# Kernel tuning notes

Hardware: AMD Instinct MI355X
Metric: run time of the kernel (lower is better)

## Reference

```python
import jax, jax.numpy as jnp
import numpy as np

B, N, C = 4, 1024, 768
H = 12
D = C // H
SCALE = D ** -0.5


def setup_inputs() -> dict:
    key = jax.random.key(0)
    k1, k2, k3, k4, k5 = jax.random.split(key, 5)
    inp = {
        'input': jax.random.normal(k1, (B, N, C), dtype=jnp.float32),
        'input_jvp': jax.random.normal(k2, (B, N, C), dtype=jnp.float32),
        # qkv linear (no bias), proj linear (with bias), torch Linear layout [out, in]
        'W_qkv': jax.random.normal(k3, (3 * C, C), dtype=jnp.float32) * (C ** -0.5),
        'W_proj': jax.random.normal(k4, (C, C), dtype=jnp.float32) * (C ** -0.5),
        'b_proj': jax.random.normal(k5, (C,), dtype=jnp.float32) * 0.02,
    }
    return inp


def _split_heads(t):
    t = t.reshape(B, N, 3, H, D).transpose(2, 0, 3, 1, 4)
    return t[0], t[1], t[2]


def reference(input, input_jvp, W_qkv, W_proj, b_proj):
    # LinearLinear: primal gets full affine, tangent gets linear part only
    qkv = jnp.einsum('bnc,oc->bno', input, W_qkv)
    qkv_jvp = jnp.einsum('bnc,oc->bno', input_jvp, W_qkv)
    q, k, v = _split_heads(qkv)
    q_jvp, k_jvp, v_jvp = _split_heads(qkv_jvp)

    q = q * SCALE
    attn = jax.nn.softmax(jnp.einsum('bhnd,bhmd->bhnm', q, k), axis=-1)
    x = jnp.einsum('bhnm,bhmd->bhnd', attn, v)

    q_jvp = q_jvp * SCALE
    A_jvp = jnp.einsum('bhnd,bhmd->bhnm', q_jvp, k)
    B_jvp = jnp.einsum('bhnd,bhmd->bhnm', q, k_jvp)
    C_jvp = jnp.einsum('bhnm,bhmd->bhnd', attn, v_jvp)
    dm_by_dr = A_jvp + B_jvp
    # softmax JVP: attn * (dm - rowsum(dm * attn))
    attn_filter_1 = dm_by_dr * attn
    row = jnp.sum(dm_by_dr * attn, axis=-1, keepdims=True)  # = diag(dm @ attn^T)
    attn_filter = attn_filter_1 - row * attn
    x_jvp = jnp.einsum('bhnm,bhmd->bhnd', attn_filter, v) + C_jvp

    x = x.transpose(0, 2, 1, 3).reshape(B, N, C)
    x_jvp = x_jvp.transpose(0, 2, 1, 3).reshape(B, N, C)

    x = jnp.einsum('bnc,oc->bno', x, W_proj) + b_proj
    x_jvp = jnp.einsum('bnc,oc->bno', x_jvp, W_proj)
    return (x, x_jvp)
```

## Files before the change

### kernel.cpp

```cpp
#include <hip/hip_runtime.h>

constexpr int Bn = 4;
constexpr int Nn = 1024;
constexpr int Cn = 768;
constexpr int Hn = 12;
constexpr int Dn = 64;
constexpr float SCALE_Q = 0.125f;
constexpr int SEG = Bn * Nn * Cn;
constexpr int NDn = Nn * Dn;
constexpr int WQ_ELE = 3 * Cn * Cn;
constexpr int WP_ELE = Cn * Cn;

typedef __attribute__((ext_vector_type(8))) short bf16x8;
typedef __attribute__((ext_vector_type(4))) float f32x4;

__device__ __forceinline__ unsigned short f2bf(float f) {
    union { float f; unsigned u; } v; v.f = f;
    unsigned r = v.u + 0x7fffu + ((v.u >> 16) & 1u);
    return (unsigned short)(r >> 16);
}
__device__ __forceinline__ float bf2f(unsigned short b) {
    union { unsigned u; float f; } v; v.u = ((unsigned)b) << 16;
    return v.f;
}
__device__ __forceinline__ bf16x8 ldfrag(const unsigned short* base, int boff) {
    return *(const bf16x8*)((const char*)base + boff);
}
#define MFMA(a, b, c) __builtin_amdgcn_mfma_f32_16x16x32_bf16((a), (b), (c), 0, 0, 0)


__global__ __launch_bounds__(256)
void conv_k(const float* __restrict__ a0, const float* __restrict__ a1,
            unsigned short* __restrict__ dst)
{
    const int P = SEG / 4;
    const int j = blockIdx.x * 256 + threadIdx.x;
    const int arr = j / P;
    const int i = (j - arr * P) * 4;
    const float* __restrict__ src = arr ? a1 : a0;
    const float4 f = *(const float4*)(src + i);
    const float ff[4] = {f.x, f.y, f.z, f.w};
    ushort4 h, lo;
#pragma unroll
    for (int t = 0; t < 4; ++t) {
        const unsigned short hv = f2bf(ff[t]);
        (&h.x)[t] = hv;
        (&lo.x)[t] = f2bf(ff[t] - bf2f(hv));
    }
    *(ushort4*)(dst + (size_t)(2 * arr) * SEG + i) = h;
    *(ushort4*)(dst + (size_t)(2 * arr + 1) * SEG + i) = lo;
}

__global__ __launch_bounds__(256)
void conv_w(const float* __restrict__ src, unsigned short* __restrict__ dh,
            unsigned short* __restrict__ dl)
{
    const int i = (blockIdx.x * 256 + threadIdx.x) * 4;
    const float4 f = *(const float4*)(src + i);
    const float ff[4] = {f.x, f.y, f.z, f.w};
    ushort4 h, lo;
#pragma unroll
    for (int t = 0; t < 4; ++t) {
        const unsigned short hv = f2bf(ff[t]);
        (&h.x)[t] = hv;
        (&lo.x)[t] = f2bf(ff[t] - bf2f(hv));
    }
    *(ushort4*)(dh + i) = h;
    *(ushort4*)(dl + i) = lo;
}

template<int MODE>
__global__ __launch_bounds__(256, 2)
void gemm_mfma(const unsigned short* __restrict__ Abase,
               const unsigned short* __restrict__ Wh,
               const unsigned short* __restrict__ Wl,
               const float* __restrict__ bias,
               unsigned short* __restrict__ qkv, float* __restrict__ out)
{
    __shared__ unsigned short sAh[128 * 64];
    __shared__ unsigned short sAl[128 * 64];
    __shared__ unsigned short sBh[128 * 64];
    __shared__ unsigned short sBl[128 * 64];

    const int tid = threadIdx.x;
    const int z = blockIdx.z;
    const int row0 = blockIdx.y << 7;
    const int col0 = blockIdx.x << 7;
    const int l = tid & 63, w = tid >> 6;
    const int wr = w >> 1, wc = w & 1;
    const int h4 = l >> 4, l15 = l & 15;
    const int sw = (l15 & 7) << 4;
    const int srow = tid >> 3;
    const int ss = tid & 7;

    const unsigned short* __restrict__ Ah = Abase + (size_t)(2 * z) * SEG;
    const unsigned short* __restrict__ Al = Abase + (size_t)(2 * z + 1) * SEG;

    f32x4 acc[4][4];
#pragma unroll
    for (int m = 0; m < 4; ++m)
#pragma unroll
        for (int n = 0; n < 4; ++n)
            acc[m][n] = (f32x4){0.f, 0.f, 0.f, 0.f};

    bf16x8 pAh[4], pAl[4], pBh[4], pBl[4];

#define G_LOADT(K0_) {                                                        \
    _Pragma("unroll")                                                         \
    for (int it = 0; it < 4; ++it) {                                          \
        const int row = srow + 32 * it;                                       \
        const size_t goA = (size_t)(row0 + row) * Cn + (K0_) + 8 * ss;        \
        const size_t goB = (size_t)(col0 + row) * Cn + (K0_) + 8 * ss;        \
        pAh[it] = *(const bf16x8*)(Ah + goA);                                 \
        pAl[it] = *(const bf16x8*)(Al + goA);                                 \
        pBh[it] = *(const bf16x8*)(Wh + goB);                                 \
        pBl[it] = *(const bf16x8*)(Wl + goB);                                 \
    } }

    G_LOADT(0);

    for (int k0 = 0; k0 < Cn; k0 += 64) {
        __syncthreads();
#pragma unroll
        for (int it = 0; it < 4; ++it) {
            const int row = srow + 32 * it;
            const int boff = row * 128 + ((ss ^ (row & 7)) << 4);
            *(bf16x8*)((char*)sAh + boff) = pAh[it];
            *(bf16x8*)((char*)sAl + boff) = pAl[it];
            *(bf16x8*)((char*)sBh + boff) = pBh[it];
            *(bf16x8*)((char*)sBl + boff) = pBl[it];
        }
        const int kn = (k0 + 64 < Cn) ? k0 + 64 : 0;
        G_LOADT(kn);
        __syncthreads();
#pragma unroll
        for (int c = 0; c < 2; ++c) {
            bf16x8 ah[4], al[4], bh[4], bl[4];
#pragma unroll
            for (int m = 0; m < 4; ++m) {
                const int boff = (64 * wr + 16 * m + l15) * 128 + ((((c << 2) | h4) << 4) ^ sw);
                ah[m] = ldfrag(sAh, boff);
                al[m] = ldfrag(sAl, boff);
            }
#pragma unroll
            for (int n = 0; n < 4; ++n) {
                const int boff = (64 * wc + 16 * n + l15) * 128 + ((((c << 2) | h4) << 4) ^ sw);
                bh[n] = ldfrag(sBh, boff);
                bl[n] = ldfrag(sBl, boff);
            }
#pragma unroll
            for (int m = 0; m < 4; ++m)
#pragma unroll
                for (int n = 0; n < 4; ++n) {
                    acc[m][n] = MFMA(ah[m], bh[n], acc[m][n]);
                    acc[m][n] = MFMA(ah[m], bl[n], acc[m][n]);
                    acc[m][n] = MFMA(al[m], bh[n], acc[m][n]);
                }
        }
    }

    if (MODE == 0) {
#pragma unroll
        for (int n = 0; n < 4; ++n) {
            const int colb = col0 + 64 * wc + 16 * n;
            const int t = colb / Cn;
            const int rem = colb - t * Cn;
            const int hh = rem >> 6;
            const int d = (rem & 63) + l15;
            const float sc = (t == 0) ? SCALE_Q : 1.0f;
            const int t2 = t + 3 * z;
            unsigned short* __restrict__ dh = qkv + (size_t)(2 * t2) * SEG;
            unsigned short* __restrict__ dl = dh + SEG;
#pragma unroll
            for (int m = 0; m < 4; ++m)
#pragma unroll
                for (int r = 0; r < 4; ++r) {
                    const int row = row0 + 64 * wr + 16 * m + 4 * h4 + r;
                    const int b = row >> 10, nq = row & 1023;
                    const size_t ad = (size_t)(b * Hn + hh) * NDn +
                        (t == 2 ? (size_t)d * Nn + nq
                                : (size_t)nq * 64 + d);
                    const float vv = acc[m][n][r] * sc;
                    const unsigned short hv = f2bf(vv);
                    dh[ad] = hv;
                    dl[ad] = f2bf(vv - bf2f(hv));
                }
        }
    } else {
#pragma unroll
        for (int n = 0; n < 4; ++n) {
            const int col = col0 + 64 * wc + 16 * n + l15;
            const float bi = (z == 0) ? bias[col] : 0.0f;
#pragma unroll
            for (int m = 0; m < 4; ++m)
#pragma unroll
                for (int r = 0; r < 4; ++r) {
                    const int row = row0 + 64 * wr + 16 * m + 4 * h4 + r;
                    out[(size_t)z * SEG + (size_t)row * Cn + col] = acc[m][n][r] + bi;
                }
        }
    }
}

__global__ __launch_bounds__(256, 2)
void attn_mfma(unsigned short* __restrict__ wsu)
{
    __shared__ unsigned short sKV[4][64 * 64];
    __shared__ unsigned short sP[4][4][16 * 64];

    const int tid = threadIdx.x;
    const int l = tid & 63;
    const int w = tid >> 6;
    const int h4 = l >> 4;
    const int l15 = l & 15;
    const int sw = (l15 & 7) << 4;
    const int rA = tid >> 3;
    const int ss = tid & 7;
    const int rB = rA + 32;

    const int bh = blockIdx.x;
    const int r0 = blockIdx.y << 6;

    const unsigned short* __restrict__ Bq = wsu + 4 * (size_t)SEG + (size_t)bh * NDn;
    const unsigned short* __restrict__ qh   = Bq;
    const unsigned short* __restrict__ kh   = Bq + 2 * (size_t)SEG;
    const unsigned short* __restrict__ vth  = Bq + 4 * (size_t)SEG;
    const unsigned short* __restrict__ qjh  = Bq + 6 * (size_t)SEG;
    const unsigned short* __restrict__ kjh  = Bq + 8 * (size_t)SEG;
    const unsigned short* __restrict__ vjth = Bq + 10 * (size_t)SEG;

    bf16x8 qhi[2], qlo[2], qjhi[2], qjlo[2];
    {
        const int qrow = r0 + w * 16 + l15;
#pragma unroll
        for (int c = 0; c < 2; ++c) {
            const size_t o = (size_t)qrow * 64 + c * 32 + h4 * 8;
            qhi[c] = *(const bf16x8*)(qh + o);
            qlo[c] = *(const bf16x8*)(qh + SEG + o);
            qjhi[c] = *(const bf16x8*)(qjh + o);
            qjlo[c] = *(const bf16x8*)(qjh + SEG + o);
        }
    }

    f32x4 mold = {-3.0e38f, -3.0e38f, -3.0e38f, -3.0e38f};
    f32x4 l_run = {0.f, 0.f, 0.f, 0.f};
    f32x4 ar_run = {0.f, 0.f, 0.f, 0.f};
    f32x4 ax[4], ac[4], ad[4];
#pragma unroll
    for (int ds = 0; ds < 4; ++ds) {
        ax[ds] = (f32x4){0.f, 0.f, 0.f, 0.f};
        ac[ds] = (f32x4){0.f, 0.f, 0.f, 0.f};
        ad[ds] = (f32x4){0.f, 0.f, 0.f, 0.f};
    }

    bf16x8 kr0[4], kr1[4], vr0[4], vr1[4];
    const int ba = rA * 128 + ((ss ^ (rA & 7)) << 4);
    const int bb = rB * 128 + ((ss ^ (rA & 7)) << 4);

#define A_LOADK(JT_) {                                                         \
    const size_t ga = (size_t)((JT_) + rA) * 64 + 8 * ss;                      \
    const size_t gb = (size_t)((JT_) + rB) * 64 + 8 * ss;                      \
    kr0[0] = *(const bf16x8*)(kh + ga);        kr1[0] = *(const bf16x8*)(kh + gb); \
    kr0[1] = *(const bf16x8*)(kh + SEG + ga);  kr1[1] = *(const bf16x8*)(kh + SEG + gb); \
    kr0[2] = *(const bf16x8*)(kjh + ga);       kr1[2] = *(const bf16x8*)(kjh + gb); \
    kr0[3] = *(const bf16x8*)(kjh + SEG + ga); kr1[3] = *(const bf16x8*)(kjh + SEG + gb); }

#define A_LOADV(JT_) {                                                         \
    const size_t ga = (size_t)rA * Nn + (JT_) + 8 * ss;                        \
    const size_t gb = (size_t)rB * Nn + (JT_) + 8 * ss;                        \
    vr0[0] = *(const bf16x8*)(vth + ga);        vr1[0] = *(const bf16x8*)(vth + gb); \
    vr0[1] = *(const bf16x8*)(vth + SEG + ga);  vr1[1] = *(const bf16x8*)(vth + SEG + gb); \
    vr0[2] = *(const bf16x8*)(vjth + ga);       vr1[2] = *(const bf16x8*)(vjth + gb); \
    vr0[3] = *(const bf16x8*)(vjth + SEG + ga); vr1[3] = *(const bf16x8*)(vjth + SEG + gb); }

#define A_WRITE(R0_, R1_) {                                                    \
    *(bf16x8*)((char*)sKV[0] + ba) = R0_[0]; *(bf16x8*)((char*)sKV[0] + bb) = R1_[0]; \
    *(bf16x8*)((char*)sKV[1] + ba) = R0_[1]; *(bf16x8*)((char*)sKV[1] + bb) = R1_[1]; \
    *(bf16x8*)((char*)sKV[2] + ba) = R0_[2]; *(bf16x8*)((char*)sKV[2] + bb) = R1_[2]; \
    *(bf16x8*)((char*)sKV[3] + ba) = R0_[3]; *(bf16x8*)((char*)sKV[3] + bb) = R1_[3]; }

    A_LOADK(0);

    for (int jt = 0; jt < Nn; jt += 64) {
        __syncthreads();
        A_WRITE(kr0, kr1);
        __syncthreads();

        f32x4 S[4], DM[4];
        __builtin_amdgcn_s_setprio(1);
#pragma unroll
        for (int kt = 0; kt < 4; ++kt) {
            f32x4 s = {0.f, 0.f, 0.f, 0.f};
            f32x4 dm = {0.f, 0.f, 0.f, 0.f};
#pragma unroll
            for (int c = 0; c < 2; ++c) {
                const int boff = (l15 + (kt << 4)) * 128 + (((h4 << 4) | (c << 6)) ^ sw);
                const bf16x8 khi = ldfrag(sKV[0], boff);
                const bf16x8 klo = ldfrag(sKV[1], boff);
                const bf16x8 jhi = ldfrag(sKV[2], boff);
                const bf16x8 jlo = ldfrag(sKV[3], boff);
                s = MFMA(qhi[c], khi, s);
                s = MFMA(qhi[c], klo, s);
                s = MFMA(qlo[c], khi, s);
                dm = MFMA(qjhi[c], khi, dm);
                dm = MFMA(qjhi[c], klo, dm);
                dm = MFMA(qjlo[c], khi, dm);
                dm = MFMA(qhi[c], jhi, dm);
                dm = MFMA(qhi[c], jlo, dm);
                dm = MFMA(qlo[c], jhi, dm);
            }
            S[kt] = s; DM[kt] = dm;
        }
        __builtin_amdgcn_s_setprio(0);

        A_LOADV(jt);
        A_LOADK((jt + 64) & (Nn - 1));

        f32x4 tmax, mnew, alpha;
#pragma unroll
        for (int r = 0; r < 4; ++r)
            tmax[r] = fmaxf(fmaxf(S[0][r], S[1][r]), fmaxf(S[2][r], S[3][r]));
#pragma unroll
        for (int m = 1; m < 16; m <<= 1)
#pragma unroll
            for (int r = 0; r < 4; ++r)
                tmax[r] = fmaxf(tmax[r], __shfl_xor(tmax[r], m));
#pragma unroll
        for (int r = 0; r < 4; ++r) {
            mnew[r] = fmaxf(mold[r], tmax[r]);
            alpha[r] = __expf(mold[r] - mnew[r]);
            mold[r] = mnew[r];
        }
        f32x4 lsum = {0.f, 0.f, 0.f, 0.f};
        f32x4 arsum = {0.f, 0.f, 0.f, 0.f};
#pragma unroll
        for (int kt = 0; kt < 4; ++kt) {
            const int key = (kt << 4) + l15;
#pragma unroll
            for (int r = 0; r < 4; ++r) {
                const float p = __expf(S[kt][r] - mnew[r]);
                const float pd = p * DM[kt][r];
                lsum[r] += p;
                arsum[r] += pd;
                const int qq = (h4 << 2) + r;
                const int boff = qq * 128 +
                    (((key & 7) << 1) | ((((key >> 3) ^ (qq & 7)) << 4)));
                const unsigned short ph = f2bf(p);
                const unsigned short pdh = f2bf(pd);
                *(unsigned short*)((char*)sP[w][0] + boff) = ph;
                *(unsigned short*)((char*)sP[w][1] + boff) = f2bf(p - bf2f(ph));
                *(unsigned short*)((char*)sP[w][2] + boff) = pdh;
                *(unsigned short*)((char*)sP[w][3] + boff) = f2bf(pd - bf2f(pdh));
            }
        }
#pragma unroll
        for (int r = 0; r < 4; ++r) {
            l_run[r] = l_run[r] * alpha[r] + lsum[r];
            ar_run[r] = ar_run[r] * alpha[r] + arsum[r];
        }
#pragma unroll
        for (int ds = 0; ds < 4; ++ds) {
            ax[ds] *= alpha; ac[ds] *= alpha; ad[ds] *= alpha;
        }

        __syncthreads();
        A_WRITE(vr0, vr1);
        __syncthreads();

        __builtin_amdgcn_s_setprio(1);
#pragma unroll
        for (int kc = 0; kc < 2; ++kc) {
            const int pxo = ((h4 << 4) | (kc << 6)) ^ sw;
            const bf16x8 phi = ldfrag(sP[w][0], l15 * 128 + pxo);
            const bf16x8 plo = ldfrag(sP[w][1], l15 * 128 + pxo);
            const bf16x8 dhi = ldfrag(sP[w][2], l15 * 128 + pxo);
            const bf16x8 dlo = ldfrag(sP[w][3], l15 * 128 + pxo);
#pragma unroll
            for (int ds = 0; ds < 4; ++ds) {
                const int boff = (l15 + (ds << 4)) * 128 + pxo;
                const bf16x8 vhi = ldfrag(sKV[0], boff);
                const bf16x8 vlo = ldfrag(sKV[1], boff);
                const bf16x8 wjh = ldfrag(sKV[2], boff);
                const bf16x8 wjl = ldfrag(sKV[3], boff);
                ax[ds] = MFMA(phi, vhi, ax[ds]);
                ax[ds] = MFMA(phi, vlo, ax[ds]);
                ax[ds] = MFMA(plo, vhi, ax[ds]);
                ac[ds] = MFMA(phi, wjh, ac[ds]);
                ac[ds] = MFMA(phi, wjl, ac[ds]);
                ac[ds] = MFMA(plo, wjh, ac[ds]);
                ad[ds] = MFMA(dhi, vhi, ad[ds]);
                ad[ds] = MFMA(dhi, vlo, ad[ds]);
                ad[ds] = MFMA(dlo, vhi, ad[ds]);
            }
        }
        __builtin_amdgcn_s_setprio(0);
    }

#pragma unroll
    for (int m = 1; m < 16; m <<= 1)
#pragma unroll
        for (int r = 0; r < 4; ++r) {
            l_run[r] += __shfl_xor(l_run[r], m);
            ar_run[r] += __shfl_xor(ar_run[r], m);
        }
    const int b = bh / Hn;
    const int hh = bh - b * Hn;
    unsigned short* __restrict__ xh = wsu;
    unsigned short* __restrict__ xl = wsu + (size_t)SEG;
    unsigned short* __restrict__ xjh = wsu + 2 * (size_t)SEG;
    unsigned short* __restrict__ xjl = wsu + 3 * (size_t)SEG;
#pragma unroll
    for (int r = 0; r < 4; ++r) {
        const int qg = r0 + w * 16 + (h4 << 2) + r;
        const float invl = 1.0f / l_run[r];
        const float rowv = ar_run[r] * invl;
        const size_t base = ((size_t)(b * Nn + qg)) * Cn + hh * Dn + l15;
#pragma unroll
        for (int ds = 0; ds < 4; ++ds) {
            const float x = ax[ds][r] * invl;
            const float xjv = fmaf(-rowv, x, (ad[ds][r] + ac[ds][r]) * invl);
            const size_t ad2 = base + ds * 16;
            const unsigned short h0 = f2bf(x);
            xh[ad2] = h0;
            xl[ad2] = f2bf(x - bf2f(h0));
            const unsigned short h1 = f2bf(xjv);
            xjh[ad2] = h1;
            xjl[ad2] = f2bf(xjv - bf2f(h1));
        }
    }
}

extern "C" void kernel_launch(void* const* d_in, const int* in_sizes, int n_in,
                              void* d_out, int out_size, void* d_ws, size_t ws_size,
                              hipStream_t stream)
{
    const float* input  = (const float*)d_in[0];
    const float* inputj = (const float*)d_in[1];
    const float* W_qkv  = (const float*)d_in[2];
    const float* W_proj = (const float*)d_in[3];
    const float* b_proj = (const float*)d_in[4];
    float* out = (float*)d_out;
    unsigned short* wsu = (unsigned short*)d_ws;
    unsigned short* regA = wsu;
    unsigned short* regB = wsu + 4 * (size_t)SEG;
    unsigned short* wqh = (unsigned short*)d_out;
    unsigned short* wql = wqh + (size_t)WQ_ELE;
    unsigned short* wph = regB;
    unsigned short* wpl = wph + (size_t)WP_ELE;

    conv_k<<<2 * (SEG / 4) / 256, 256, 0, stream>>>(input, inputj, regA);
    conv_w<<<(WQ_ELE / 4) / 256, 256, 0, stream>>>(W_qkv, wqh, wql);
    gemm_mfma<0><<<dim3(18, 32, 2), 256, 0, stream>>>(regA, wqh, wql, nullptr,
                                                      regB, nullptr);
    attn_mfma<<<dim3(48, 16), 256, 0, stream>>>(wsu);
    conv_w<<<(WP_ELE / 4) / 256, 256, 0, stream>>>(W_proj, wph, wpl);
    gemm_mfma<1><<<dim3(6, 32, 2), 256, 0, stream>>>(regA, wph, wpl, b_proj,
                                                     nullptr, out);
}
```

Baseline: 398.5 us.

## Enlarge GEMM tiles to 256x256 with 512-thread blocks and K-step 32

Restructures the split-bf16 GEMM kernel from 128x128 tiles with 256 threads and K-step 64 to 256x256 tiles with 512 threads (8 waves, each computing 128x64) and K-step 32, with a new LDS swizzle. This raises arithmetic intensity per global load and halves the number of blocks. The cost is more accumulator registers per thread (128 floats), which may hurt occupancy or cause spills. The smaller grid (288 and 96 blocks) may also underfill the GPU's compute units, especially for the projection GEMM.

After: 485.5 us. 21.8% more time.

```diff
diff --git a/kernel.cpp b/kernel.cpp
--- a/kernel.cpp
+++ b/kernel.cpp
@@ -70,91 +70,93 @@
 }
 
 template<int MODE>
-__global__ __launch_bounds__(256, 2)
+__global__ __launch_bounds__(512, 2)
 void gemm_mfma(const unsigned short* __restrict__ Abase,
                const unsigned short* __restrict__ Wh,
                const unsigned short* __restrict__ Wl,
                const float* __restrict__ bias,
                unsigned short* __restrict__ qkv, float* __restrict__ out)
 {
-    __shared__ unsigned short sAh[128 * 64];
-    __shared__ unsigned short sAl[128 * 64];
-    __shared__ unsigned short sBh[128 * 64];
-    __shared__ unsigned short sBl[128 * 64];
+    __shared__ unsigned short sAh[256 * 32];
+    __shared__ unsigned short sAl[256 * 32];
+    __shared__ unsigned short sBh[256 * 32];
+    __shared__ unsigned short sBl[256 * 32];
 
     const int tid = threadIdx.x;
     const int z = blockIdx.z;
-    const int row0 = blockIdx.y << 7;
-    const int col0 = blockIdx.x << 7;
+    const int row0 = blockIdx.y << 8;
+    const int col0 = blockIdx.x << 8;
     const int l = tid & 63, w = tid >> 6;
-    const int wr = w >> 1, wc = w & 1;
+    const int wr = w >> 2, wc = w & 3;
     const int h4 = l >> 4, l15 = l & 15;
-    const int sw = (l15 & 7) << 4;
-    const int srow = tid >> 3;
-    const int ss = tid & 7;
+    const int swz = (h4 ^ (l15 & 3)) << 4;
+    const int srow = tid >> 2;
+    const int sch = tid & 3;
 
     const unsigned short* __restrict__ Ah = Abase + (size_t)(2 * z) * SEG;
     const unsigned short* __restrict__ Al = Abase + (size_t)(2 * z + 1) * SEG;
 
-    f32x4 acc[4][4];
-#pragma unroll
-    for (int m = 0; m < 4; ++m)
+    f32x4 acc[8][4];
+#pragma unroll
+    for (int m = 0; m < 8; ++m)
 #pragma unroll
         for (int n = 0; n < 4; ++n)
             acc[m][n] = (f32x4){0.f, 0.f, 0.f, 0.f};
 
-    bf16x8 pAh[4], pAl[4], pBh[4], pBl[4];
-
-#define G_LOADT(K0_) {                                                        \
-    _Pragma("unroll")                                                         \
-    for (int it = 0; it < 4; ++it) {                                          \
-        const int row = srow + 32 * it;                                       \
-        const size_t goA = (size_t)(row0 + row) * Cn + (K0_) + 8 * ss;        \
-        const size_t goB = (size_t)(col0 + row) * Cn + (K0_) + 8 * ss;        \
-        pAh[it] = *(const bf16x8*)(Ah + goA);                                 \
-        pAl[it] = *(const bf16x8*)(Al + goA);                                 \
-        pBh[it] = *(const bf16x8*)(Wh + goB);                                 \
-        pBl[it] = *(const bf16x8*)(Wl + goB);                                 \
-    } }
+    bf16x8 pA0h, pA0l, pA1h, pA1l, pB0h, pB0l, pB1h, pB1l;
+
+#define G_LOADT(K0_) {                                                         \
+    const size_t gA0 = (size_t)(row0 + srow) * Cn + (K0_) + 8 * sch;           \
+    const size_t gA1 = (size_t)(row0 + srow + 128) * Cn + (K0_) + 8 * sch;     \
+    const size_t gB0 = (size_t)(col0 + srow) * Cn + (K0_) + 8 * sch;           \
+    const size_t gB1 = (size_t)(col0 + srow + 128) * Cn + (K0_) + 8 * sch;     \
+    pA0h = *(const bf16x8*)(Ah + gA0);  pA0l = *(const bf16x8*)(Al + gA0);     \
+    pA1h = *(const bf16x8*)(Ah + gA1);  pA1l = *(const bf16x8*)(Al + gA1);     \
+    pB0h = *(const bf16x8*)(Wh + gB0);  pB0l = *(const bf16x8*)(Wl + gB0);     \
+    pB1h = *(const bf16x8*)(Wh + gB1);  pB1l = *(const bf16x8*)(Wl + gB1);     \
+    }
+
+    const int ba0 = srow * 64 + ((sch ^ (srow & 3)) << 4);
+    const int ba1 = (srow + 128) * 64 + ((sch ^ (srow & 3)) << 4);
 
     G_LOADT(0);
 
-    for (int k0 = 0; k0 < Cn; k0 += 64) {
-        __syncthreads();
-#pragma unroll
-        for (int it = 0; it < 4; ++it) {
-            const int row = srow + 32 * it;
-            const int boff = row * 128 + ((ss ^ (row & 7)) << 4);
-            *(bf16x8*)((char*)sAh + boff) = pAh[it];
-            *(bf16x8*)((char*)sAl + boff) = pAl[it];
-            *(bf16x8*)((char*)sBh + boff) = pBh[it];
-            *(bf16x8*)((char*)sBl + boff) = pBl[it];
-        }
-        const int kn = (k0 + 64 < Cn) ? k0 + 64 : 0;
+    for (int k0 = 0; k0 < Cn; k0 += 32) {
+        __syncthreads();
+        *(bf16x8*)((char*)sAh + ba0) = pA0h;  *(bf16x8*)((char*)sAl + ba0) = pA0l;
+        *(bf16x8*)((char*)sAh + ba1) = pA1h;  *(bf16x8*)((char*)sAl + ba1) = pA1l;
+        *(bf16x8*)((char*)sBh + ba0) = pB0h;  *(bf16x8*)((char*)sBl + ba0) = pB0l;
+        *(bf16x8*)((char*)sBh + ba1) = pB1h;  *(bf16x8*)((char*)sBl + ba1) = pB1l;
+        const int kn = (k0 + 32 < Cn) ? k0 + 32 : 0;
         G_LOADT(kn);
         __syncthreads();
-#pragma unroll
-        for (int c = 0; c < 2; ++c) {
-            bf16x8 ah[4], al[4], bh[4], bl[4];
-#pragma unroll
-            for (int m = 0; m < 4; ++m) {
-                const int boff = (64 * wr + 16 * m + l15) * 128 + ((((c << 2) | h4) << 4) ^ sw);
-                ah[m] = ldfrag(sAh, boff);
-                al[m] = ldfrag(sAl, boff);
+
+        bf16x8 bh[4], bl[4];
+#pragma unroll
+        for (int n = 0; n < 4; ++n) {
+            const int boff = (64 * wc + 16 * n + l15) * 64 + swz;
+            bh[n] = ldfrag(sBh, boff);
+            bl[n] = ldfrag(sBl, boff);
+        }
+#pragma unroll
+        for (int mh = 0; mh < 2; ++mh) {
+            bf16x8 ah[4], al[4];
+#pragma unroll
+            for (int mi = 0; mi < 4; ++mi) {
+                const int m = mh * 4 + mi;
+                const int boff = (128 * wr + 16 * m + l15) * 64 + swz;
+                ah[mi] = ldfrag(sAh, boff);
+                al[mi] = ldfrag(sAl, boff);
             }
 #pragma unroll
-            for (int n = 0; n < 4; ++n) {
-                const int boff = (64 * wc + 16 * n + l15) * 128 + ((((c << 2) | h4) << 4) ^ sw);
-                bh[n] = ldfrag(sBh, boff);
-                bl[n] = ldfrag(sBl, boff);
-            }
-#pragma unroll
-            for (int m = 0; m < 4; ++m)
+            for (int mi = 0; mi < 4; ++mi)
 #pragma unroll
                 for (int n = 0; n < 4; ++n) {
-                    acc[m][n] = MFMA(ah[m], bh[n], acc[m][n]);
-                    acc[m][n] = MFMA(ah[m], bl[n], acc[m][n]);
-                    acc[m][n] = MFMA(al[m], bh[n], acc[m][n]);
+                    f32x4 a = acc[mh * 4 + mi][n];
+                    a = MFMA(ah[mi], bh[n], a);
+                    a = MFMA(ah[mi], bl[n], a);
+                    a = MFMA(al[mi], bh[n], a);
+                    acc[mh * 4 + mi][n] = a;
                 }
         }
     }
@@ -172,10 +174,10 @@
             unsigned short* __restrict__ dh = qkv + (size_t)(2 * t2) * SEG;
             unsigned short* __restrict__ dl = dh + SEG;
 #pragma unroll
-            for (int m = 0; m < 4; ++m)
+            for (int m = 0; m < 8; ++m)
 #pragma unroll
                 for (int r = 0; r < 4; ++r) {
-                    const int row = row0 + 64 * wr + 16 * m + 4 * h4 + r;
+                    const int row = row0 + 128 * wr + 16 * m + 4 * h4 + r;
                     const int b = row >> 10, nq = row & 1023;
                     const size_t ad = (size_t)(b * Hn + hh) * NDn +
                         (t == 2 ? (size_t)d * Nn + nq
@@ -192,10 +194,10 @@
             const int col = col0 + 64 * wc + 16 * n + l15;
             const float bi = (z == 0) ? bias[col] : 0.0f;
 #pragma unroll
-            for (int m = 0; m < 4; ++m)
+            for (int m = 0; m < 8; ++m)
 #pragma unroll
                 for (int r = 0; r < 4; ++r) {
-                    const int row = row0 + 64 * wr + 16 * m + 4 * h4 + r;
+                    const int row = row0 + 128 * wr + 16 * m + 4 * h4 + r;
                     out[(size_t)z * SEG + (size_t)row * Cn + col] = acc[m][n][r] + bi;
                 }
         }
@@ -450,10 +452,10 @@
 
     conv_k<<<2 * (SEG / 4) / 256, 256, 0, stream>>>(input, inputj, regA);
     conv_w<<<(WQ_ELE / 4) / 256, 256, 0, stream>>>(W_qkv, wqh, wql);
-    gemm_mfma<0><<<dim3(18, 32, 2), 256, 0, stream>>>(regA, wqh, wql, nullptr,
-                                                      regB, nullptr);
+    gemm_mfma<0><<<dim3(9, 16, 2), 512, 0, stream>>>(regA, wqh, wql, nullptr,
+                                                     regB, nullptr);
     attn_mfma<<<dim3(48, 16), 256, 0, stream>>>(wsu);
     conv_w<<<(WP_ELE / 4) / 256, 256, 0, stream>>>(W_proj, wph, wpl);
-    gemm_mfma<1><<<dim3(6, 32, 2), 256, 0, stream>>>(regA, wph, wpl, b_proj,
+    gemm_mfma<1><<<dim3(3, 16, 2), 512, 0, stream>>>(regA, wph, wpl, b_proj,
                                                      nullptr, out);
 }
```
